# Kernel optimization log

Hardware: AMD Instinct MI355X
Metric: run time of the kernel (lower is better)

## Reference

```python
import jax, jax.numpy as jnp
import numpy as np

DIM = 1024
DIM_HEAD = 64
HEADS = 16
DIM_INNER = DIM_HEAD * HEADS  # 1024


def setup_inputs() -> dict:
    key = jax.random.key(0)
    k1, k2, k3 = jax.random.split(key, 3)
    b, n = 2, 2048
    x = jax.random.normal(k1, (b, n, DIM), dtype=jnp.float32)
    gamma = jnp.ones((DIM,), dtype=jnp.float32)
    # torch Linear weight [out,in] applied as x @ W.T; store pre-transposed [in,out]
    w_qkv = jax.random.normal(k2, (DIM, 3 * DIM_INNER), dtype=jnp.float32) * (DIM ** -0.5)
    w_out = jax.random.normal(k3, (DIM_INNER, DIM), dtype=jnp.float32) * (DIM_INNER ** -0.5)
    return {"x": x, "gamma": gamma, "w_qkv": w_qkv, "w_out": w_out}


def reference(x, gamma, w_qkv, w_out):
    h, d = HEADS, DIM_HEAD
    scale = d ** -0.5
    rms_scale = DIM ** 0.5
    # RMSNorm: F.normalize(x, dim=-1) * sqrt(dim) * gamma  (eps=1e-12 clamp on L2 norm)
    norm = jnp.maximum(jnp.linalg.norm(x, axis=-1, keepdims=True), 1e-12)
    xn = x / norm * rms_scale * gamma
    b, n, _ = x.shape
    qkv = xn @ w_qkv  # [b, n, 3*h*d]
    qkv = qkv.reshape(b, n, 3, h, d)
    q = qkv[:, :, 0].transpose(0, 2, 1, 3) * scale  # [b, h, n, d]
    k = qkv[:, :, 1].transpose(0, 2, 1, 3)
    v = qkv[:, :, 2].transpose(0, 2, 1, 3)
    sim = jnp.einsum('bhid,bhjd->bhij', q, k)  # [b, h, n, n]
    causal_mask = jnp.triu(jnp.ones((n, n), dtype=bool), k=1)
    neg = -jnp.finfo(sim.dtype).max
    sim = jnp.where(causal_mask, neg, sim)
    attn = jax.nn.softmax(sim, axis=-1)
    out = jnp.einsum('bhij,bhjd->bhid', attn, v)  # [b, h, n, d]
    out = out.transpose(0, 2, 1, 3).reshape(b, n, h * d)
    return out @ w_out
```

## Files before the change

### kernel.cpp

```cpp
#include <hip/hip_runtime.h>
#include <hip/hip_bf16.h>

typedef __bf16 bf16x8 __attribute__((ext_vector_type(8)));
typedef short s16x4 __attribute__((ext_vector_type(4)));
typedef float f32x4 __attribute__((ext_vector_type(4)));
typedef unsigned short u16x8 __attribute__((ext_vector_type(8)));

#define MFMA_K32(a, b, c) __builtin_amdgcn_mfma_f32_16x16x32_bf16(a, b, c, 0, 0, 0)

static __device__ __forceinline__ f32x4 mfma_k16(s16x4 a, s16x4 b, f32x4 c) {
#ifdef __HIP_DEVICE_COMPILE__
    return __builtin_amdgcn_mfma_f32_16x16x16bf16_1k(a, b, c, 0, 0, 0);
#else
    return c;
#endif
}

static __device__ __forceinline__ float fast_exp2(float x) {
#ifdef __HIP_DEVICE_COMPILE__
    return __builtin_amdgcn_exp2f(x);
#else
    return x;
#endif
}

static __device__ __forceinline__ void prio_hi() {
#ifdef __HIP_DEVICE_COMPILE__
    __builtin_amdgcn_s_setprio(1);
#endif
}
static __device__ __forceinline__ void prio_lo() {
#ifdef __HIP_DEVICE_COMPILE__
    __builtin_amdgcn_s_setprio(0);
#endif
}

#define GLL16(gp, lp)                                              \
    __builtin_amdgcn_global_load_lds(                              \
        (const __attribute__((address_space(1))) void*)(gp),       \
        (__attribute__((address_space(3))) void*)(lp), 16, 0, 0)

static __device__ __forceinline__ unsigned short f2bf(float f) {
    unsigned int u = __float_as_uint(f);
    u += 0x7fffu + ((u >> 16) & 1u);
    return (unsigned short)(u >> 16);
}

static __device__ __forceinline__ unsigned int cvtpk_bf16(float lo, float hi) {
#if defined(__HIP_DEVICE_COMPILE__) && __has_builtin(__builtin_amdgcn_cvt_pk_bf16_f32)
    typedef __bf16 bf16x2 __attribute__((ext_vector_type(2)));
    bf16x2 r = __builtin_amdgcn_cvt_pk_bf16_f32(lo, hi);
    return __builtin_bit_cast(unsigned int, r);
#else
    return (unsigned int)f2bf(lo) | ((unsigned int)f2bf(hi) << 16);
#endif
}

#define LOG2E 1.44269504088896340736f

__global__ __launch_bounds__(256) void prep_k(
    const float* __restrict__ x, const float* __restrict__ gamma,
    const float* __restrict__ w_qkv, const float* __restrict__ w_out,
    unsigned short* __restrict__ xn, unsigned short* __restrict__ wtq,
    unsigned short* __restrict__ wto) {
    __shared__ float sm[32][33];
    int bid = blockIdx.x, tid = threadIdx.x;
    if (bid < 4096) {
        const float* in;
        unsigned short* out;
        int R = 1024, C, bx, by;
        if (bid < 3072) { in = w_qkv; out = wtq; C = 3072; bx = bid % 96; by = bid / 96; }
        else { int b2 = bid - 3072; in = w_out; out = wto; C = 1024; bx = b2 % 32; by = b2 / 32; }
        int c0 = bx * 32, r0 = by * 32;
        int tr = tid >> 5, tc = tid & 31;
#pragma unroll
        for (int i = 0; i < 4; i++)
            sm[tr + i * 8][tc] = in[(size_t)(r0 + tr + i * 8) * C + c0 + tc];
        __syncthreads();
#pragma unroll
        for (int i = 0; i < 4; i++)
            out[(size_t)(c0 + tr + i * 8) * R + r0 + tc] = f2bf(sm[tc][tr + i * 8]);
    } else {
        int row = bid - 4096;
        const float* xr = x + (size_t)row * 1024;
        float4 v = *(const float4*)(xr + tid * 4);
        float ss = v.x * v.x + v.y * v.y + v.z * v.z + v.w * v.w;
#pragma unroll
        for (int off = 1; off < 64; off <<= 1) ss += __shfl_xor(ss, off, 64);
        if ((tid & 63) == 0) sm[0][tid >> 6] = ss;
        __syncthreads();
        float tot = sm[0][0] + sm[0][1] + sm[0][2] + sm[0][3];
        float f = 32.0f / fmaxf(sqrtf(tot), 1e-12f);
        float4 g = *(const float4*)(gamma + tid * 4);
        uint2 o;
        o.x = cvtpk_bf16(v.x * f * g.x, v.y * f * g.y);
        o.y = cvtpk_bf16(v.z * f * g.z, v.w * f * g.w);
        *(uint2*)(xn + (size_t)row * 1024 + tid * 4) = o;
    }
}

template <int MODE, int BM>
__global__ __launch_bounds__(256) void gemm_bt_k(
    const unsigned short* __restrict__ A, const unsigned short* __restrict__ BT,
    float* __restrict__ C, unsigned short* __restrict__ qw,
    unsigned short* __restrict__ kw, unsigned short* __restrict__ vw,
    int M, int N, int K) {
    constexpr int RT = 4;
    constexpr int CT = (BM == 128) ? 4 : 2;
    __shared__ unsigned short As[BM][32];
    __shared__ unsigned short Bs[128][32];
    int tid = threadIdx.x;
    int wave = tid >> 6, lane = tid & 63, quad = lane >> 4, l16 = lane & 15;
    int wrb, wcb;
    if constexpr (BM == 128) { wrb = (wave >> 1) * 64; wcb = (wave & 1) * 64; }
    else { wrb = 0; wcb = wave * 32; }
    int m0 = blockIdx.y * BM, n0 = blockIdx.x * 128;
    int lrow = lane >> 2, lcol = (lane & 3) * 8;
    const unsigned short *Ag0, *Ag1 = nullptr;
    if constexpr (BM == 128) {
        Ag0 = A + (size_t)(m0 + wave * 32 + lrow) * K + lcol;
        Ag1 = A + (size_t)(m0 + wave * 32 + 16 + lrow) * K + lcol;
    } else {
        Ag0 = A + (size_t)(m0 + wave * 16 + lrow) * K + lcol;
    }
    const unsigned short* Bg0 = BT + (size_t)(n0 + wave * 32 + lrow) * K + lcol;
    const unsigned short* Bg1 = BT + (size_t)(n0 + wave * 32 + 16 + lrow) * K + lcol;
    f32x4 acc[RT][CT] = {};
    for (int k0 = 0; k0 < K; k0 += 32) {
        __syncthreads();
        if constexpr (BM == 128) {
            GLL16(Ag0 + k0, &As[wave * 32][0]);
            GLL16(Ag1 + k0, &As[wave * 32 + 16][0]);
        } else {
            GLL16(Ag0 + k0, &As[wave * 16][0]);
        }
        GLL16(Bg0 + k0, &Bs[wave * 32][0]);
        GLL16(Bg1 + k0, &Bs[wave * 32 + 16][0]);
        __syncthreads();
        bf16x8 af[RT], bfr[CT];
#pragma unroll
        for (int t = 0; t < RT; t++)
            af[t] = *(const bf16x8*)&As[wrb + t * 16 + l16][quad * 8];
#pragma unroll
        for (int t = 0; t < CT; t++)
            bfr[t] = *(const bf16x8*)&Bs[wcb + t * 16 + l16][quad * 8];
#pragma unroll
        for (int rt = 0; rt < RT; rt++)
#pragma unroll
            for (int ct = 0; ct < CT; ct++)
                acc[rt][ct] = MFMA_K32(af[rt], bfr[ct], acc[rt][ct]);
    }
#pragma unroll
    for (int rt = 0; rt < RT; rt++) {
        int mb = m0 + wrb + rt * 16 + quad * 4;
        int b = mb >> 11, nn = mb & 2047;
#pragma unroll
        for (int ct = 0; ct < CT; ct++) {
            int col = n0 + wcb + ct * 16 + l16;
            if (MODE == 0) {
#pragma unroll
                for (int r = 0; r < 4; r++)
                    C[(size_t)(mb + r) * N + col] = acc[rt][ct][r];
            } else {
                int sec = col >> 10, ci = col & 1023;
                int hh = ci >> 6, dd = ci & 63;
                int bh = b * 16 + hh;
                if (sec == 0) {
#pragma unroll
                    for (int r = 0; r < 4; r++)
                        qw[((size_t)bh * 2048 + nn + r) * 64 + dd] =
                            f2bf(acc[rt][ct][r] * (0.125f * LOG2E));
                } else if (sec == 1) {
#pragma unroll
                    for (int r = 0; r < 4; r++)
                        kw[((size_t)bh * 2048 + nn + r) * 64 + dd] = f2bf(acc[rt][ct][r]);
                } else {
                    uint2 pk;
                    pk.x = cvtpk_bf16(acc[rt][ct][0], acc[rt][ct][1]);
                    pk.y = cvtpk_bf16(acc[rt][ct][2], acc[rt][ct][3]);
                    *(uint2*)&vw[((size_t)bh * 64 + dd) * 2048 + nn] = pk;
                }
            }
        }
    }
}

__global__ __launch_bounds__(512, 4) void attn_k(
    const unsigned short* __restrict__ q, const unsigned short* __restrict__ k,
    const unsigned short* __restrict__ vt, unsigned short* __restrict__ o) {
    __shared__ __align__(16) char smem[38912];
    typedef unsigned short ush;
    ush(*Ks)[2][32][72] = (ush(*)[2][32][72])smem;
    ush(*Vt)[2][64][40] = (ush(*)[2][64][40])(smem + 18432);
    float(*Osm)[68] = (float(*)[68])smem;
    float* msm = (float*)(smem + 18432);
    float* lsm = msm + 64;

    int bh = blockIdx.x;
    int qt = 31 - (int)blockIdx.y;
    int tid = threadIdx.x, wave = tid >> 6, lane = tid & 63;
    int quad = lane >> 4, l16 = lane & 15;
    int g = wave >> 2, wq = wave & 3;
    int b = bh >> 4, h = bh & 15;
    const ush* qg = q + (size_t)bh * 2048 * 64;
    const ush* kg = k + (size_t)bh * 2048 * 64;
    const ush* vg = vt + (size_t)bh * 64 * 2048;

    int ti = wq * 64 + lane;
    int kr = ti >> 3, kc = (ti & 7) * 8;
    int vr = ti >> 2, vc = (ti & 3) * 8;
    const ush* Kg = kg + (size_t)kr * 64 + kc;
    const ush* Vg = vg + (size_t)vr * 2048 + vc;

    int row_l = wq * 16 + l16;
    int q0w = qt * 64 + wq * 16;
    bf16x8 bq[2];
#pragma unroll
    for (int ks = 0; ks < 2; ks++)
        bq[ks] = *(const bf16x8*)&qg[(size_t)(q0w + l16) * 64 + ks * 32 + quad * 8];

    f32x4 ot[4] = {};
    float mrun = -1e30f, lrun = 0.f;
    int nT = qt + 1;
    int kt0 = g ? (qt + 1) : 0;

    u16x8 pk, pv;
    pk = *(const u16x8*)(Kg + (size_t)kt0 * 2048);
    pv = *(const u16x8*)(Vg + kt0 * 32);
    *(u16x8*)&Ks[g][0][kr][kc] = pk;
    *(u16x8*)&Vt[g][0][vr][vc] = pv;
    __syncthreads();

    for (int i = 0; i < nT; i++) {
        int cb = i & 1, kt = kt0 + i;
        bool pf = (i + 1 < nT);
        if (pf) {
            pk = *(const u16x8*)(Kg + (size_t)(kt + 1) * 2048);
            pv = *(const u16x8*)(Vg + (kt + 1) * 32);
        }
        f32x4 sf[2];
        prio_hi();
#pragma unroll
        for (int ct = 0; ct < 2; ct++) {
            bf16x8 ak0 = *(const bf16x8*)&Ks[g][cb][ct * 16 + l16][quad * 8];
            bf16x8 ak1 = *(const bf16x8*)&Ks[g][cb][ct * 16 + l16][32 + quad * 8];
            f32x4 s = {};
            s = MFMA_K32(ak0, bq[0], s);
            s = MFMA_K32(ak1, bq[1], s);
            sf[ct] = s;
        }
        prio_lo();
        if (kt >= 2 * qt) {
#pragma unroll
            for (int ct = 0; ct < 2; ct++)
#pragma unroll
                for (int r = 0; r < 4; r++)
                    if (kt * 32 + ct * 16 + quad * 4 + r > qt * 64 + row_l)
                        sf[ct][r] = -1e30f;
        }
        float m0 = fmaxf(fmaxf(sf[0][0], sf[0][1]), fmaxf(sf[0][2], sf[0][3]));
        float m1 = fmaxf(fmaxf(sf[1][0], sf[1][1]), fmaxf(sf[1][2], sf[1][3]));
        float mx = fmaxf(m0, m1);
        mx = fmaxf(mx, __shfl_xor(mx, 16, 64));
        mx = fmaxf(mx, __shfl_xor(mx, 32, 64));
        if (mx > mrun + 8.0f) {
            float al = fast_exp2(mrun - mx);
            mrun = mx;
#pragma unroll
            for (int dt = 0; dt < 4; dt++)
#pragma unroll
                for (int r = 0; r < 4; r++) ot[dt][r] *= al;
        }
        float rs = 0.f;
#pragma unroll
        for (int ct = 0; ct < 2; ct++)
#pragma unroll
            for (int r = 0; r < 4; r++) {
                float p = fast_exp2(sf[ct][r] - mrun);
                sf[ct][r] = p;
                rs += p;
            }
        rs += __shfl_xor(rs, 16, 64);
        rs += __shfl_xor(rs, 32, 64);
        lrun += rs;
        s16x4 bpr[2];
#pragma unroll
        for (int ct = 0; ct < 2; ct++) {
            uint2 u;
            u.x = cvtpk_bf16(sf[ct][0], sf[ct][1]);
            u.y = cvtpk_bf16(sf[ct][2], sf[ct][3]);
            bpr[ct] = __builtin_bit_cast(s16x4, u);
        }
        prio_hi();
#pragma unroll
        for (int dt = 0; dt < 4; dt++)
#pragma unroll
            for (int ct = 0; ct < 2; ct++) {
                s16x4 av = *(const s16x4*)&Vt[g][cb][dt * 16 + l16][ct * 16 + quad * 4];
                ot[dt] = mfma_k16(av, bpr[ct], ot[dt]);
            }
        prio_lo();
        if (pf) {
            *(u16x8*)&Ks[g][1 - cb][kr][kc] = pk;
            *(u16x8*)&Vt[g][1 - cb][vr][vc] = pv;
        }
        __syncthreads();
    }

    if (g == 1) {
        msm[row_l] = mrun;
        lsm[row_l] = lrun;
#pragma unroll
        for (int dt = 0; dt < 4; dt++)
            *(f32x4*)&Osm[row_l][dt * 16 + quad * 4] = ot[dt];
    }
    __syncthreads();
    if (g == 0) {
        float m1 = msm[row_l], l1 = lsm[row_l];
        float mmax = fmaxf(mrun, m1);
        float a0 = fast_exp2(mrun - mmax), a1 = fast_exp2(m1 - mmax);
        float inv = 1.0f / (a0 * lrun + a1 * l1);
        float s0 = a0 * inv, s1 = a1 * inv;
        size_t rowbase = ((size_t)b * 2048 + qt * 64 + row_l) * 1024 + h * 64;
#pragma unroll
        for (int dt = 0; dt < 4; dt++) {
            f32x4 o1 = *(const f32x4*)&Osm[row_l][dt * 16 + quad * 4];
            uint2 pkk;
            pkk.x = cvtpk_bf16(ot[dt][0] * s0 + o1[0] * s1,
                               ot[dt][1] * s0 + o1[1] * s1);
            pkk.y = cvtpk_bf16(ot[dt][2] * s0 + o1[2] * s1,
                               ot[dt][3] * s0 + o1[3] * s1);
            *(uint2*)&o[rowbase + dt * 16 + quad * 4] = pkk;
        }
    }
}

extern "C" void kernel_launch(void* const* d_in, const int* in_sizes, int n_in,
                              void* d_out, int out_size, void* d_ws, size_t ws_size,
                              hipStream_t stream) {
    const float* x = (const float*)d_in[0];
    const float* gamma = (const float*)d_in[1];
    const float* w_qkv = (const float*)d_in[2];
    const float* w_out = (const float*)d_in[3];
    float* out = (float*)d_out;
    char* ws = (char*)d_ws;

    unsigned short* xn = (unsigned short*)(ws);
    unsigned short* wtq = (unsigned short*)(ws + 8388608);
    unsigned short* wto = (unsigned short*)(ws + 14680064);
    unsigned short* qw = (unsigned short*)(ws + 16777216);
    unsigned short* kw = (unsigned short*)(ws + 25165824);
    unsigned short* vw = (unsigned short*)(ws + 33554432);
    unsigned short* ao = xn;

    prep_k<<<8192, 256, 0, stream>>>(x, gamma, w_qkv, w_out, xn, wtq, wto);
    gemm_bt_k<1, 128><<<dim3(24, 32), 256, 0, stream>>>(xn, wtq, nullptr, qw, kw, vw,
                                                        4096, 3072, 1024);
    attn_k<<<dim3(32, 32), 512, 0, stream>>>(qw, kw, vw, ao);
    gemm_bt_k<0, 64><<<dim3(8, 64), 256, 0, stream>>>(ao, wto, out, nullptr, nullptr,
                                                      nullptr, 4096, 1024, 1024);
}
```

Baseline: 191.7 us.

## Drop LDS staging in attention; per-wave direct global K/V loads with finer causal bounds

Rewrites the attention kernel so each wave independently processes 16 query rows, loading K and V fragments directly from global memory instead of double-buffered shared memory with block-wide barriers. The two-group KV split and its shared-memory merge are removed, and each wave iterates only up to its own causal limit, cutting masked work. The row-sum reduction is deferred to the end and lrun is rescaled with the running max. This trades barrier and LDS overhead for redundant global/L2 traffic across waves and unhidden load latency.

```diff
diff --git a/kernel.cpp b/kernel.cpp
--- a/kernel.cpp
+++ b/kernel.cpp
@@ -185,78 +185,65 @@
     }
 }
 
-__global__ __launch_bounds__(512, 4) void attn_k(
+__global__ __launch_bounds__(256, 4) void attn_k(
     const unsigned short* __restrict__ q, const unsigned short* __restrict__ k,
     const unsigned short* __restrict__ vt, unsigned short* __restrict__ o) {
-    __shared__ __align__(16) char smem[38912];
     typedef unsigned short ush;
-    ush(*Ks)[2][32][72] = (ush(*)[2][32][72])smem;
-    ush(*Vt)[2][64][40] = (ush(*)[2][64][40])(smem + 18432);
-    float(*Osm)[68] = (float(*)[68])smem;
-    float* msm = (float*)(smem + 18432);
-    float* lsm = msm + 64;
-
     int bh = blockIdx.x;
-    int qt = 31 - (int)blockIdx.y;
+    int sg = 31 - (int)blockIdx.y;
     int tid = threadIdx.x, wave = tid >> 6, lane = tid & 63;
     int quad = lane >> 4, l16 = lane & 15;
-    int g = wave >> 2, wq = wave & 3;
+    int s = sg * 4 + wave;
+    int q0 = s * 16;
     int b = bh >> 4, h = bh & 15;
     const ush* qg = q + (size_t)bh * 2048 * 64;
     const ush* kg = k + (size_t)bh * 2048 * 64;
     const ush* vg = vt + (size_t)bh * 64 * 2048;
 
-    int ti = wq * 64 + lane;
-    int kr = ti >> 3, kc = (ti & 7) * 8;
-    int vr = ti >> 2, vc = (ti & 3) * 8;
-    const ush* Kg = kg + (size_t)kr * 64 + kc;
-    const ush* Vg = vg + (size_t)vr * 2048 + vc;
-
-    int row_l = wq * 16 + l16;
-    int q0w = qt * 64 + wq * 16;
     bf16x8 bq[2];
 #pragma unroll
     for (int ks = 0; ks < 2; ks++)
-        bq[ks] = *(const bf16x8*)&qg[(size_t)(q0w + l16) * 64 + ks * 32 + quad * 8];
+        bq[ks] = *(const bf16x8*)&qg[(size_t)(q0 + l16) * 64 + ks * 32 + quad * 8];
 
     f32x4 ot[4] = {};
     float mrun = -1e30f, lrun = 0.f;
-    int nT = qt + 1;
-    int kt0 = g ? (qt + 1) : 0;
-
-    u16x8 pk, pv;
-    pk = *(const u16x8*)(Kg + (size_t)kt0 * 2048);
-    pv = *(const u16x8*)(Vg + kt0 * 32);
-    *(u16x8*)&Ks[g][0][kr][kc] = pk;
-    *(u16x8*)&Vt[g][0][vr][vc] = pv;
-    __syncthreads();
-
-    for (int i = 0; i < nT; i++) {
-        int cb = i & 1, kt = kt0 + i;
-        bool pf = (i + 1 < nT);
-        if (pf) {
-            pk = *(const u16x8*)(Kg + (size_t)(kt + 1) * 2048);
-            pv = *(const u16x8*)(Vg + (kt + 1) * 32);
-        }
+    int nfull = q0 >> 5;
+
+    const ush* kb = kg + (size_t)l16 * 64 + quad * 8;
+    const ush* vb = vg + (size_t)l16 * 2048 + quad * 4;
+
+    for (int t = 0; t <= nfull; t++) {
+        const ush* kt_p = kb + (size_t)t * 32 * 64;
+        bf16x8 kf0a = *(const bf16x8*)(kt_p);
+        bf16x8 kf0b = *(const bf16x8*)(kt_p + 32);
+        bf16x8 kf1a = *(const bf16x8*)(kt_p + 16 * 64);
+        bf16x8 kf1b = *(const bf16x8*)(kt_p + 16 * 64 + 32);
+        s16x4 vf[4][2];
+#pragma unroll
+        for (int dt = 0; dt < 4; dt++)
+#pragma unroll
+            for (int ct = 0; ct < 2; ct++)
+                vf[dt][ct] = *(const s16x4*)(vb + (size_t)dt * 16 * 2048 + t * 32 + ct * 16);
         f32x4 sf[2];
         prio_hi();
-#pragma unroll
-        for (int ct = 0; ct < 2; ct++) {
-            bf16x8 ak0 = *(const bf16x8*)&Ks[g][cb][ct * 16 + l16][quad * 8];
-            bf16x8 ak1 = *(const bf16x8*)&Ks[g][cb][ct * 16 + l16][32 + quad * 8];
-            f32x4 s = {};
-            s = MFMA_K32(ak0, bq[0], s);
-            s = MFMA_K32(ak1, bq[1], s);
-            sf[ct] = s;
+        {
+            f32x4 s0 = {};
+            s0 = MFMA_K32(kf0a, bq[0], s0);
+            s0 = MFMA_K32(kf0b, bq[1], s0);
+            sf[0] = s0;
+            f32x4 s1 = {};
+            s1 = MFMA_K32(kf1a, bq[0], s1);
+            s1 = MFMA_K32(kf1b, bq[1], s1);
+            sf[1] = s1;
         }
         prio_lo();
-        if (kt >= 2 * qt) {
+        if (t == nfull) {
+            int qrow = q0 + l16;
 #pragma unroll
             for (int ct = 0; ct < 2; ct++)
 #pragma unroll
                 for (int r = 0; r < 4; r++)
-                    if (kt * 32 + ct * 16 + quad * 4 + r > qt * 64 + row_l)
-                        sf[ct][r] = -1e30f;
+                    if (t * 32 + ct * 16 + quad * 4 + r > qrow) sf[ct][r] = -1e30f;
         }
         float m0 = fmaxf(fmaxf(sf[0][0], sf[0][1]), fmaxf(sf[0][2], sf[0][3]));
         float m1 = fmaxf(fmaxf(sf[1][0], sf[1][1]), fmaxf(sf[1][2], sf[1][3]));
@@ -266,6 +253,7 @@
         if (mx > mrun + 8.0f) {
             float al = fast_exp2(mrun - mx);
             mrun = mx;
+            lrun *= al;
 #pragma unroll
             for (int dt = 0; dt < 4; dt++)
 #pragma unroll
@@ -280,8 +268,6 @@
                 sf[ct][r] = p;
                 rs += p;
             }
-        rs += __shfl_xor(rs, 16, 64);
-        rs += __shfl_xor(rs, 32, 64);
         lrun += rs;
         s16x4 bpr[2];
 #pragma unroll
@@ -295,43 +281,20 @@
 #pragma unroll
         for (int dt = 0; dt < 4; dt++)
 #pragma unroll
-            for (int ct = 0; ct < 2; ct++) {
-                s16x4 av = *(const s16x4*)&Vt[g][cb][dt * 16 + l16][ct * 16 + quad * 4];
-                ot[dt] = mfma_k16(av, bpr[ct], ot[dt]);
-            }
+            for (int ct = 0; ct < 2; ct++)
+                ot[dt] = mfma_k16(vf[dt][ct], bpr[ct], ot[dt]);
         prio_lo();
-        if (pf) {
-            *(u16x8*)&Ks[g][1 - cb][kr][kc] = pk;
-            *(u16x8*)&Vt[g][1 - cb][vr][vc] = pv;
-        }
-        __syncthreads();
-    }
-
-    if (g == 1) {
-        msm[row_l] = mrun;
-        lsm[row_l] = lrun;
-#pragma unroll
-        for (int dt = 0; dt < 4; dt++)
-            *(f32x4*)&Osm[row_l][dt * 16 + quad * 4] = ot[dt];
-    }
-    __syncthreads();
-    if (g == 0) {
-        float m1 = msm[row_l], l1 = lsm[row_l];
-        float mmax = fmaxf(mrun, m1);
-        float a0 = fast_exp2(mrun - mmax), a1 = fast_exp2(m1 - mmax);
-        float inv = 1.0f / (a0 * lrun + a1 * l1);
-        float s0 = a0 * inv, s1 = a1 * inv;
-        size_t rowbase = ((size_t)b * 2048 + qt * 64 + row_l) * 1024 + h * 64;
-#pragma unroll
-        for (int dt = 0; dt < 4; dt++) {
-            f32x4 o1 = *(const f32x4*)&Osm[row_l][dt * 16 + quad * 4];
-            uint2 pkk;
-            pkk.x = cvtpk_bf16(ot[dt][0] * s0 + o1[0] * s1,
-                               ot[dt][1] * s0 + o1[1] * s1);
-            pkk.y = cvtpk_bf16(ot[dt][2] * s0 + o1[2] * s1,
-                               ot[dt][3] * s0 + o1[3] * s1);
-            *(uint2*)&o[rowbase + dt * 16 + quad * 4] = pkk;
-        }
+    }
+    lrun += __shfl_xor(lrun, 16, 64);
+    lrun += __shfl_xor(lrun, 32, 64);
+    float inv = 1.0f / lrun;
+    size_t rowbase = ((size_t)b * 2048 + q0 + l16) * 1024 + h * 64;
+#pragma unroll
+    for (int dt = 0; dt < 4; dt++) {
+        uint2 pk;
+        pk.x = cvtpk_bf16(ot[dt][0] * inv, ot[dt][1] * inv);
+        pk.y = cvtpk_bf16(ot[dt][2] * inv, ot[dt][3] * inv);
+        *(uint2*)&o[rowbase + dt * 16 + quad * 4] = pk;
     }
 }
 
@@ -356,7 +319,7 @@
     prep_k<<<8192, 256, 0, stream>>>(x, gamma, w_qkv, w_out, xn, wtq, wto);
     gemm_bt_k<1, 128><<<dim3(24, 32), 256, 0, stream>>>(xn, wtq, nullptr, qw, kw, vw,
                                                         4096, 3072, 1024);
-    attn_k<<<dim3(32, 32), 512, 0, stream>>>(qw, kw, vw, ao);
+    attn_k<<<dim3(32, 32), 256, 0, stream>>>(qw, kw, vw, ao);
     gemm_bt_k<0, 64><<<dim3(8, 64), 256, 0, stream>>>(ao, wto, out, nullptr, nullptr,
                                                       nullptr, 4096, 1024, 1024);
 }
```

After: 352.5 us. 1.84x slower.
